# Kernel optimization log

Hardware: AMD Instinct MI355X
Metric: run time of the kernel (lower is better)

The kernel has to match this reference:

```python
import jax, jax.numpy as jnp
import numpy as np

N = 1024
C = 256

def setup_inputs() -> dict:
    key = jax.random.key(0)
    k1, k2, k3 = jax.random.split(key, 3)
    x = jax.random.normal(k1, (N, C), dtype=jnp.float32)
    # nn.Linear(channels, 1): weight (1, channels) -> store as (channels,), bias scalar
    w = jax.random.normal(k2, (C,), dtype=jnp.float32) * (1.0 / np.sqrt(C))
    b = jax.random.normal(k3, (1,), dtype=jnp.float32) * 0.01
    return {"x": x, "w": w, "b": b}

def reference(x, w, b):
    # pairwise broadcast-add: pair[i, j, c] = x[j, c] + x[i, c]  (matches x[None,:] + x[:, None])
    pair = x[None, :, :] + x[:, None, :]          # [n, n, c]
    z = jnp.einsum('ijc,c->ij', pair, w) + b[0]    # linear gate -> [n, n]
    out = jnp.einsum('ijc,ij->ic', pair, z)        # gated weighted sum over j -> [n, c]
    return out
```

## Files before the change

### kernel.cpp

```cpp
#include <hip/hip_runtime.h>

#define N 1024
#define C 256
#define NB1 32
#define ROWS1 (N / NB1)
#define NB2 128
#define ROWS2 (N / NB2)

__global__ void phase1(const float* __restrict__ x, const float* __restrict__ w,
                       float* __restrict__ s, float* __restrict__ S1p,
                       float* __restrict__ S2p, float* __restrict__ Tp) {
    __shared__ float s_lds[ROWS1];
    const int b    = blockIdx.x;
    const int r0   = b * ROWS1;
    const int wave = threadIdx.x >> 6;
    const int lane = threadIdx.x & 63;

    const float4* wv = reinterpret_cast<const float4*>(w);
    const float4  wf = wv[lane];

    #pragma unroll
    for (int k = 0; k < ROWS1 / 4; ++k) {
        const int lrow = wave * (ROWS1 / 4) + k;
        const int row  = r0 + lrow;
        const float4 xv = reinterpret_cast<const float4*>(x + row * C)[lane];
        float acc = xv.x * wf.x + xv.y * wf.y + xv.z * wf.z + xv.w * wf.w;
        #pragma unroll
        for (int off = 32; off > 0; off >>= 1)
            acc += __shfl_down(acc, off, 64);
        if (lane == 0) { s_lds[lrow] = acc; s[row] = acc; }
    }
    __syncthreads();

    const int c = threadIdx.x;
    float p1 = 0.f, p2 = 0.f;
    #pragma unroll 4
    for (int j = 0; j < ROWS1; ++j) {
        const float xv = x[(r0 + j) * C + c];
        const float sj = s_lds[j];
        p1 += xv;
        p2 += xv * sj;
    }
    S1p[b * C + c] = p1;
    S2p[b * C + c] = p2;

    if (threadIdx.x == 0) {
        float t = 0.f;
        #pragma unroll
        for (int j = 0; j < ROWS1; ++j) t += s_lds[j];
        Tp[b] = t;
    }
}

__global__ void phase2(const float* __restrict__ x, const float* __restrict__ s,
                       const float* __restrict__ S1p, const float* __restrict__ S2p,
                       const float* __restrict__ Tp, const float* __restrict__ bptr,
                       float* __restrict__ out) {
    const int c = threadIdx.x;
    float S1 = 0.f, S2 = 0.f;
    #pragma unroll
    for (int p = 0; p < NB1; ++p) {
        S1 += S1p[p * C + c];
        S2 += S2p[p * C + c];
    }
    float T = 0.f;
    #pragma unroll
    for (int p = 0; p < NB1; ++p) T += Tp[p];

    const float bb = bptr[0];
    const int  r0 = blockIdx.x * ROWS2;
    #pragma unroll
    for (int k = 0; k < ROWS2; ++k) {
        const int   i  = r0 + k;
        const float sb = s[i] + bb;
        const float xv = x[i * C + c];
        out[i * C + c] = sb * S1 + S2 + xv * ((float)N * sb + T);
    }
}

extern "C" void kernel_launch(void* const* d_in, const int* in_sizes, int n_in,
                              void* d_out, int out_size, void* d_ws, size_t ws_size,
                              hipStream_t stream) {
    const float* x = (const float*)d_in[0];
    const float* w = (const float*)d_in[1];
    const float* b = (const float*)d_in[2];
    float* out = (float*)d_out;

    float* s   = (float*)d_ws;
    float* S1p = s + N;
    float* S2p = S1p + NB1 * C;
    float* Tp  = S2p + NB1 * C;

    phase1<<<NB1, 256, 0, stream>>>(x, w, s, S1p, S2p, Tp);
    phase2<<<NB2, 256, 0, stream>>>(x, s, S1p, S2p, Tp, b, out);
}
```

Measured before the change: 13.46 us.

## Fuse two phases into one cooperative kernel with grid-wide sync

Merges the partial-sum phase and the output phase into a single cooperative kernel of 64 blocks that synchronises with a grid barrier instead of a second launch. Each block keeps its row dot products in LDS and reuses them for its own output rows, so the global s array is no longer written or read back. This removes one kernel launch and a global round trip. In exchange it adds the cost of a cooperative grid sync, and every block must now reduce 64 partials instead of 32.

```diff
diff --git a/kernel.cpp b/kernel.cpp
--- a/kernel.cpp
+++ b/kernel.cpp
@@ -1,41 +1,44 @@
 #include <hip/hip_runtime.h>
+#include <hip/hip_cooperative_groups.h>
+
+namespace cg = cooperative_groups;
 
 #define N 1024
 #define C 256
-#define NB1 32
-#define ROWS1 (N / NB1)
-#define NB2 128
-#define ROWS2 (N / NB2)
+#define NB 64
+#define ROWS (N / NB)
 
-__global__ void phase1(const float* __restrict__ x, const float* __restrict__ w,
-                       float* __restrict__ s, float* __restrict__ S1p,
-                       float* __restrict__ S2p, float* __restrict__ Tp) {
-    __shared__ float s_lds[ROWS1];
+__global__ void fused(const float* __restrict__ x, const float* __restrict__ w,
+                      const float* __restrict__ bptr, float* __restrict__ out,
+                      float* __restrict__ ws) {
+    float* S1p = ws;
+    float* S2p = S1p + NB * C;
+    float* Tp  = S2p + NB * C;
+
+    __shared__ float s_lds[ROWS];
     const int b    = blockIdx.x;
-    const int r0   = b * ROWS1;
+    const int r0   = b * ROWS;
     const int wave = threadIdx.x >> 6;
     const int lane = threadIdx.x & 63;
 
-    const float4* wv = reinterpret_cast<const float4*>(w);
-    const float4  wf = wv[lane];
+    const float4 wf = reinterpret_cast<const float4*>(w)[lane];
 
     #pragma unroll
-    for (int k = 0; k < ROWS1 / 4; ++k) {
-        const int lrow = wave * (ROWS1 / 4) + k;
-        const int row  = r0 + lrow;
-        const float4 xv = reinterpret_cast<const float4*>(x + row * C)[lane];
+    for (int k = 0; k < ROWS / 4; ++k) {
+        const int lrow = wave * (ROWS / 4) + k;
+        const float4 xv = reinterpret_cast<const float4*>(x + (r0 + lrow) * C)[lane];
         float acc = xv.x * wf.x + xv.y * wf.y + xv.z * wf.z + xv.w * wf.w;
         #pragma unroll
         for (int off = 32; off > 0; off >>= 1)
             acc += __shfl_down(acc, off, 64);
-        if (lane == 0) { s_lds[lrow] = acc; s[row] = acc; }
+        if (lane == 0) s_lds[lrow] = acc;
     }
     __syncthreads();
 
     const int c = threadIdx.x;
     float p1 = 0.f, p2 = 0.f;
-    #pragma unroll 4
-    for (int j = 0; j < ROWS1; ++j) {
+    #pragma unroll
+    for (int j = 0; j < ROWS; ++j) {
         const float xv = x[(r0 + j) * C + c];
         const float sj = s_lds[j];
         p1 += xv;
@@ -43,36 +46,30 @@
     }
     S1p[b * C + c] = p1;
     S2p[b * C + c] = p2;
-
     if (threadIdx.x == 0) {
         float t = 0.f;
         #pragma unroll
-        for (int j = 0; j < ROWS1; ++j) t += s_lds[j];
+        for (int j = 0; j < ROWS; ++j) t += s_lds[j];
         Tp[b] = t;
     }
-}
 
-__global__ void phase2(const float* __restrict__ x, const float* __restrict__ s,
-                       const float* __restrict__ S1p, const float* __restrict__ S2p,
-                       const float* __restrict__ Tp, const float* __restrict__ bptr,
-                       float* __restrict__ out) {
-    const int c = threadIdx.x;
+    cg::this_grid().sync();
+
     float S1 = 0.f, S2 = 0.f;
-    #pragma unroll
-    for (int p = 0; p < NB1; ++p) {
+    #pragma unroll 8
+    for (int p = 0; p < NB; ++p) {
         S1 += S1p[p * C + c];
         S2 += S2p[p * C + c];
     }
     float T = 0.f;
-    #pragma unroll
-    for (int p = 0; p < NB1; ++p) T += Tp[p];
+    #pragma unroll 8
+    for (int p = 0; p < NB; ++p) T += Tp[p];
 
     const float bb = bptr[0];
-    const int  r0 = blockIdx.x * ROWS2;
     #pragma unroll
-    for (int k = 0; k < ROWS2; ++k) {
+    for (int k = 0; k < ROWS; ++k) {
         const int   i  = r0 + k;
-        const float sb = s[i] + bb;
+        const float sb = s_lds[k] + bb;
         const float xv = x[i * C + c];
         out[i * C + c] = sb * S1 + S2 + xv * ((float)N * sb + T);
     }
@@ -85,12 +82,8 @@
     const float* w = (const float*)d_in[1];
     const float* b = (const float*)d_in[2];
     float* out = (float*)d_out;
+    float* ws  = (float*)d_ws;
 
-    float* s   = (float*)d_ws;
-    float* S1p = s + N;
-    float* S2p = S1p + NB1 * C;
-    float* Tp  = S2p + NB1 * C;
-
-    phase1<<<NB1, 256, 0, stream>>>(x, w, s, S1p, S2p, Tp);
-    phase2<<<NB2, 256, 0, stream>>>(x, s, S1p, S2p, Tp, b, out);
+    void* args[] = { (void*)&x, (void*)&w, (void*)&b, (void*)&out, (void*)&ws };
+    hipLaunchCooperativeKernel((void*)fused, dim3(NB), dim3(256), args, 0, stream);
 }
```

Result: slower. 37.47 us (+178.4%).
